# Kernel optimization log

Hardware: AMD Instinct MI355X
Metric: run time of the kernel (lower is better)

## Reference

```python
import jax, jax.numpy as jnp
import numpy as np
import math

B, C, H, W = 16, 1, 1536, 1536


def setup_inputs() -> dict:
    key = jax.random.key(0)
    x = jax.random.normal(key, (B, C, H, W), dtype=jnp.float32)
    return {"inputs": x}


def _remove_nan(v):
    # utils.remove_nan: replace NaNs with zeros
    return jnp.where(jnp.isnan(v), jnp.zeros_like(v), v)


def reference(inputs):
    # Vectorized over batch; tf.map_fn applied axes 1,2 per-sample, which are
    # axes 2,3 (H, W) of the full (B, C, H, W) tensor.
    grad = lambda m, ax: jnp.roll(m, 1, axis=ax) - m
    p = grad(inputs, 2)          # d/dH
    q = grad(inputs, 3)          # d/dW
    r = grad(p, 2)               # d2/dH2
    s = grad(p, 3)               # d2/dHdW
    t = grad(q, 3)               # d2/dW2

    one_pq = 1.0 + p * p + q * q
    # mean curvature
    Hc = _remove_nan(-((1.0 + q * q) * r - 2.0 * p * q * s + (1.0 + p * p) * t)
                     / (2.0 * jnp.sqrt(one_pq ** 3)))
    # gaussian curvature
    Kc = _remove_nan((r * t - s * s) / (one_pq ** 2))

    root = jnp.sqrt(Hc * Hc - Kc)
    k_min = _remove_nan(Hc - root)
    k_max = _remove_nan(Hc + root)

    si = _remove_nan((2.0 / math.pi) * jnp.arctan((k_max + k_min) / (k_max - k_min)))
    return si
```

## Files before the change

### kernel.cpp

```cpp
#include <hip/hip_runtime.h>
#include <cmath>

#define B_ 16
#define H_ 1536
#define W_ 1536

typedef float v4f __attribute__((ext_vector_type(4)));

__global__ __launch_bounds__(384) void ShapeIndex_kernel(
        const float* __restrict__ x, float* __restrict__ out) {
#pragma clang fp contract(off)
    const int hraw = blockIdx.x;
    const int h  = (hraw & 7) * (H_ / 8) + (hraw >> 3);
    const int b  = blockIdx.y;
    const int w  = threadIdx.x * 4;

    const float* plane = x + (size_t)b * (H_ * W_);
    const int hm1 = (h == 0) ? (H_ - 1) : (h - 1);
    const int hm2 = (h <= 1) ? (h + H_ - 2) : (h - 2);

    const float4 vc = *(const float4*)(plane + h   * W_ + w);
    const float4 v1 = *(const float4*)(plane + hm1 * W_ + w);
    const float4 v2 = *(const float4*)(plane + hm2 * W_ + w);

    const int wm1 = (w == 0) ? (W_ - 1) : (w - 1);
    const int wm2 = (w == 0) ? (W_ - 2) : (w - 2);
    const float L0  = plane[h   * W_ + wm1];
    const float L1  = plane[h   * W_ + wm2];
    const float Lh1 = plane[hm1 * W_ + wm1];

    const v4f xc    = {vc.x, vc.y, vc.z, vc.w};
    const v4f xh1   = {v1.x, v1.y, v1.z, v1.w};
    const v4f xh2   = {v2.x, v2.y, v2.z, v2.w};
    const v4f xw1   = {L0,  vc.x, vc.y, vc.z};
    const v4f xw2   = {L1,  L0,  vc.x, vc.y};
    const v4f xh1w1 = {Lh1, v1.x, v1.y, v1.z};

    const v4f p    = xh1   - xc;
    const v4f q    = xw1   - xc;
    const v4f p_up = xh2   - xh1;
    const v4f p_lf = xh1w1 - xw1;
    const v4f q_lf = xw2   - xw1;
    const v4f r = p_up - p;
    const v4f s = p_lf - p;
    const v4f t = q_lf - q;

    const v4f pp = p * p;
    const v4f qq = q * q;
    const v4f one_pq = (1.0f + pp) + qq;
    const v4f A = ((1.0f + qq) * r - ((2.0f * p) * q) * s) + (1.0f + pp) * t;
    const v4f numk = r * t - s * s;

    v4f rsqv;
#pragma unroll
    for (int j = 0; j < 4; ++j)
        rsqv[j] = __builtin_amdgcn_rsqf(one_pq[j]);
    const v4f i2 = rsqv * rsqv;
    const v4f i3 = i2 * rsqv;
    const v4f i4 = i2 * i2;
    const v4f halfA = -0.5f * A;
    v4f Hc = halfA * i3;
    v4f Kc = numk * i4;
    const v4f HH = Hc * Hc;
    v4f disc = HH - Kc;

    v4f mag;
#pragma unroll
    for (int j = 0; j < 4; ++j) mag[j] = HH[j] + __builtin_fabsf(Kc[j]);
    const v4f thr = mag * 0x1p-16f;
    bool need[4];
    bool any = false;
#pragma unroll
    for (int j = 0; j < 4; ++j) {
        need[j] = __builtin_fabsf(disc[j]) <= thr[j];
        any |= need[j];
    }
    if (__builtin_expect(any, 0)) {
#pragma unroll
        for (int j = 0; j < 4; ++j) if (need[j]) {
            const float sqj  = one_pq[j] * one_pq[j];
            const float cubj = sqj * one_pq[j];
            const float se  = __builtin_sqrtf(cubj);
            const float hce = -(A[j] / (2.0f * se));
            const float kce = numk[j] / sqj;
            Hc[j]   = hce;
            disc[j] = hce * hce - kce;
        }
    }

    v4f root;
#pragma unroll
    for (int j = 0; j < 4; ++j) root[j] = __builtin_amdgcn_sqrtf(disc[j]);

    v4f u;
    bool big[4];
#pragma unroll
    for (int j = 0; j < 4; ++j) {
        const float aH = __builtin_fabsf(Hc[j]);
        big[j] = aH > root[j];
        const float mn = big[j] ? root[j] : aH;
        const float mx = big[j] ? aH : root[j];
        u[j] = mn * __builtin_amdgcn_rcpf(mx);
    }

    const v4f x2 = u * u;
    const v4f C5 = -0.01172120f, C4 = 0.05265332f, C3 = -0.11643287f,
              C2 = 0.19354346f,  C1 = -0.33262347f, C0 = 0.99997726f;
    v4f pl = __builtin_elementwise_fma(x2, C5, C4);
    pl = __builtin_elementwise_fma(x2, pl, C3);
    pl = __builtin_elementwise_fma(x2, pl, C2);
    pl = __builtin_elementwise_fma(x2, pl, C1);
    pl = __builtin_elementwise_fma(x2, pl, C0);
    const v4f a    = u * pl;
    const v4f asub = 1.57079632679489662f - a;

    v4f rs;
#pragma unroll
    for (int j = 0; j < 4; ++j)
        rs[j] = __builtin_copysignf(big[j] ? asub[j] : a[j], Hc[j]);
    const v4f siv = 0.63661977236758134f * rs;

    float res[4];
#pragma unroll
    for (int j = 0; j < 4; ++j)
        res[j] = (siv[j] == siv[j]) ? siv[j] : 0.0f;

    *(float4*)(out + (size_t)b * (H_ * W_) + h * W_ + w) =
        make_float4(res[0], res[1], res[2], res[3]);
}

extern "C" void kernel_launch(void* const* d_in, const int* in_sizes, int n_in,
                              void* d_out, int out_size, void* d_ws, size_t ws_size,
                              hipStream_t stream) {
    const float* x = (const float*)d_in[0];
    float* out = (float*)d_out;
    dim3 grid(H_, B_);
    dim3 block(384);
    ShapeIndex_kernel<<<grid, block, 0, stream>>>(x, out);
}
```

Baseline: 255.8 us.

## Process four rows per block to reuse vertical stencil loads

Each block now computes four consecutive output rows, loading six input rows once into registers and sharing them across the rows' stencils, and the grid shrinks by four. This cuts redundant global loads (previously each row reloaded its two upper neighbours plus the scalar left-halo values), which should help a memory-bound stencil. The cost is more registers per thread and fewer blocks in flight, which may lower occupancy and latency hiding; the scalar halo loads are still unvectorised.

```diff
diff --git a/kernel.cpp b/kernel.cpp
--- a/kernel.cpp
+++ b/kernel.cpp
@@ -10,123 +10,141 @@
 __global__ __launch_bounds__(384) void ShapeIndex_kernel(
         const float* __restrict__ x, float* __restrict__ out) {
 #pragma clang fp contract(off)
-    const int hraw = blockIdx.x;
-    const int h  = (hraw & 7) * (H_ / 8) + (hraw >> 3);
+    const int graw = blockIdx.x;
+    const int g  = (graw & 7) * (384 / 8) + (graw >> 3);
+    const int h0 = g * 4;
     const int b  = blockIdx.y;
     const int w  = threadIdx.x * 4;
 
     const float* plane = x + (size_t)b * (H_ * W_);
-    const int hm1 = (h == 0) ? (H_ - 1) : (h - 1);
-    const int hm2 = (h <= 1) ? (h + H_ - 2) : (h - 2);
+    const int rm1 = (h0 == 0) ? H_ - 1 : h0 - 1;
+    const int rm2 = (h0 == 0) ? H_ - 2 : h0 - 2;
 
-    const float4 vc = *(const float4*)(plane + h   * W_ + w);
-    const float4 v1 = *(const float4*)(plane + hm1 * W_ + w);
-    const float4 v2 = *(const float4*)(plane + hm2 * W_ + w);
+    const int rows[6] = {rm2, rm1, h0, h0 + 1, h0 + 2, h0 + 3};
+
+    float4 R[6];
+#pragma unroll
+    for (int i = 0; i < 6; ++i)
+        R[i] = *(const float4*)(plane + (size_t)rows[i] * W_ + w);
 
     const int wm1 = (w == 0) ? (W_ - 1) : (w - 1);
     const int wm2 = (w == 0) ? (W_ - 2) : (w - 2);
-    const float L0  = plane[h   * W_ + wm1];
-    const float L1  = plane[h   * W_ + wm2];
-    const float Lh1 = plane[hm1 * W_ + wm1];
+    float Lw1[6], Lw2[6];
+#pragma unroll
+    for (int i = 1; i < 6; ++i) Lw1[i] = plane[(size_t)rows[i] * W_ + wm1];
+#pragma unroll
+    for (int i = 2; i < 6; ++i) Lw2[i] = plane[(size_t)rows[i] * W_ + wm2];
 
-    const v4f xc    = {vc.x, vc.y, vc.z, vc.w};
-    const v4f xh1   = {v1.x, v1.y, v1.z, v1.w};
-    const v4f xh2   = {v2.x, v2.y, v2.z, v2.w};
-    const v4f xw1   = {L0,  vc.x, vc.y, vc.z};
-    const v4f xw2   = {L1,  L0,  vc.x, vc.y};
-    const v4f xh1w1 = {Lh1, v1.x, v1.y, v1.z};
+    float* const oplane = out + (size_t)b * (H_ * W_);
 
-    const v4f p    = xh1   - xc;
-    const v4f q    = xw1   - xc;
-    const v4f p_up = xh2   - xh1;
-    const v4f p_lf = xh1w1 - xw1;
-    const v4f q_lf = xw2   - xw1;
-    const v4f r = p_up - p;
-    const v4f s = p_lf - p;
-    const v4f t = q_lf - q;
+#pragma unroll
+    for (int rr = 0; rr < 4; ++rr) {
+        const float4 vc = R[2 + rr];
+        const float4 v1 = R[1 + rr];
+        const float4 v2 = R[0 + rr];
+        const float L0  = Lw1[2 + rr];
+        const float L1  = Lw2[2 + rr];
+        const float Lh1 = Lw1[1 + rr];
 
-    const v4f pp = p * p;
-    const v4f qq = q * q;
-    const v4f one_pq = (1.0f + pp) + qq;
-    const v4f A = ((1.0f + qq) * r - ((2.0f * p) * q) * s) + (1.0f + pp) * t;
-    const v4f numk = r * t - s * s;
+        const v4f xc    = {vc.x, vc.y, vc.z, vc.w};
+        const v4f xh1   = {v1.x, v1.y, v1.z, v1.w};
+        const v4f xh2   = {v2.x, v2.y, v2.z, v2.w};
+        const v4f xw1   = {L0,  vc.x, vc.y, vc.z};
+        const v4f xw2   = {L1,  L0,  vc.x, vc.y};
+        const v4f xh1w1 = {Lh1, v1.x, v1.y, v1.z};
 
-    v4f rsqv;
+        const v4f p    = xh1   - xc;
+        const v4f q    = xw1   - xc;
+        const v4f p_up = xh2   - xh1;
+        const v4f p_lf = xh1w1 - xw1;
+        const v4f q_lf = xw2   - xw1;
+        const v4f r = p_up - p;
+        const v4f s = p_lf - p;
+        const v4f t = q_lf - q;
+
+        const v4f pp = p * p;
+        const v4f qq = q * q;
+        const v4f one_pq = (1.0f + pp) + qq;
+        const v4f A = ((1.0f + qq) * r - ((2.0f * p) * q) * s) + (1.0f + pp) * t;
+        const v4f numk = r * t - s * s;
+
+        v4f rsqv;
 #pragma unroll
-    for (int j = 0; j < 4; ++j)
-        rsqv[j] = __builtin_amdgcn_rsqf(one_pq[j]);
-    const v4f i2 = rsqv * rsqv;
-    const v4f i3 = i2 * rsqv;
-    const v4f i4 = i2 * i2;
-    const v4f halfA = -0.5f * A;
-    v4f Hc = halfA * i3;
-    v4f Kc = numk * i4;
-    const v4f HH = Hc * Hc;
-    v4f disc = HH - Kc;
+        for (int j = 0; j < 4; ++j)
+            rsqv[j] = __builtin_amdgcn_rsqf(one_pq[j]);
+        const v4f i2 = rsqv * rsqv;
+        const v4f i3 = i2 * rsqv;
+        const v4f i4 = i2 * i2;
+        const v4f halfA = -0.5f * A;
+        v4f Hc = halfA * i3;
+        v4f Kc = numk * i4;
+        const v4f HH = Hc * Hc;
+        v4f disc = HH - Kc;
 
-    v4f mag;
+        v4f mag;
 #pragma unroll
-    for (int j = 0; j < 4; ++j) mag[j] = HH[j] + __builtin_fabsf(Kc[j]);
-    const v4f thr = mag * 0x1p-16f;
-    bool need[4];
-    bool any = false;
+        for (int j = 0; j < 4; ++j) mag[j] = HH[j] + __builtin_fabsf(Kc[j]);
+        const v4f thr = mag * 0x1p-16f;
+        bool need[4];
+        bool any = false;
 #pragma unroll
-    for (int j = 0; j < 4; ++j) {
-        need[j] = __builtin_fabsf(disc[j]) <= thr[j];
-        any |= need[j];
+        for (int j = 0; j < 4; ++j) {
+            need[j] = __builtin_fabsf(disc[j]) <= thr[j];
+            any |= need[j];
+        }
+        if (__builtin_expect(any, 0)) {
+#pragma unroll
+            for (int j = 0; j < 4; ++j) if (need[j]) {
+                const float sqj  = one_pq[j] * one_pq[j];
+                const float cubj = sqj * one_pq[j];
+                const float se  = __builtin_sqrtf(cubj);
+                const float hce = -(A[j] / (2.0f * se));
+                const float kce = numk[j] / sqj;
+                Hc[j]   = hce;
+                disc[j] = hce * hce - kce;
+            }
+        }
+
+        v4f root;
+#pragma unroll
+        for (int j = 0; j < 4; ++j) root[j] = __builtin_amdgcn_sqrtf(disc[j]);
+
+        v4f u;
+        bool big[4];
+#pragma unroll
+        for (int j = 0; j < 4; ++j) {
+            const float aH = __builtin_fabsf(Hc[j]);
+            big[j] = aH > root[j];
+            const float mn = big[j] ? root[j] : aH;
+            const float mx = big[j] ? aH : root[j];
+            u[j] = mn * __builtin_amdgcn_rcpf(mx);
+        }
+
+        const v4f x2 = u * u;
+        const v4f C5 = -0.01172120f, C4 = 0.05265332f, C3 = -0.11643287f,
+                  C2 = 0.19354346f,  C1 = -0.33262347f, C0 = 0.99997726f;
+        v4f pl = __builtin_elementwise_fma(x2, C5, C4);
+        pl = __builtin_elementwise_fma(x2, pl, C3);
+        pl = __builtin_elementwise_fma(x2, pl, C2);
+        pl = __builtin_elementwise_fma(x2, pl, C1);
+        pl = __builtin_elementwise_fma(x2, pl, C0);
+        const v4f a    = u * pl;
+        const v4f asub = 1.57079632679489662f - a;
+
+        v4f rs;
+#pragma unroll
+        for (int j = 0; j < 4; ++j)
+            rs[j] = __builtin_copysignf(big[j] ? asub[j] : a[j], Hc[j]);
+        const v4f siv = 0.63661977236758134f * rs;
+
+        float res[4];
+#pragma unroll
+        for (int j = 0; j < 4; ++j)
+            res[j] = (siv[j] == siv[j]) ? siv[j] : 0.0f;
+
+        *(float4*)(oplane + (size_t)(h0 + rr) * W_ + w) =
+            make_float4(res[0], res[1], res[2], res[3]);
     }
-    if (__builtin_expect(any, 0)) {
-#pragma unroll
-        for (int j = 0; j < 4; ++j) if (need[j]) {
-            const float sqj  = one_pq[j] * one_pq[j];
-            const float cubj = sqj * one_pq[j];
-            const float se  = __builtin_sqrtf(cubj);
-            const float hce = -(A[j] / (2.0f * se));
-            const float kce = numk[j] / sqj;
-            Hc[j]   = hce;
-            disc[j] = hce * hce - kce;
-        }
-    }
-
-    v4f root;
-#pragma unroll
-    for (int j = 0; j < 4; ++j) root[j] = __builtin_amdgcn_sqrtf(disc[j]);
-
-    v4f u;
-    bool big[4];
-#pragma unroll
-    for (int j = 0; j < 4; ++j) {
-        const float aH = __builtin_fabsf(Hc[j]);
-        big[j] = aH > root[j];
-        const float mn = big[j] ? root[j] : aH;
-        const float mx = big[j] ? aH : root[j];
-        u[j] = mn * __builtin_amdgcn_rcpf(mx);
-    }
-
-    const v4f x2 = u * u;
-    const v4f C5 = -0.01172120f, C4 = 0.05265332f, C3 = -0.11643287f,
-              C2 = 0.19354346f,  C1 = -0.33262347f, C0 = 0.99997726f;
-    v4f pl = __builtin_elementwise_fma(x2, C5, C4);
-    pl = __builtin_elementwise_fma(x2, pl, C3);
-    pl = __builtin_elementwise_fma(x2, pl, C2);
-    pl = __builtin_elementwise_fma(x2, pl, C1);
-    pl = __builtin_elementwise_fma(x2, pl, C0);
-    const v4f a    = u * pl;
-    const v4f asub = 1.57079632679489662f - a;
-
-    v4f rs;
-#pragma unroll
-    for (int j = 0; j < 4; ++j)
-        rs[j] = __builtin_copysignf(big[j] ? asub[j] : a[j], Hc[j]);
-    const v4f siv = 0.63661977236758134f * rs;
-
-    float res[4];
-#pragma unroll
-    for (int j = 0; j < 4; ++j)
-        res[j] = (siv[j] == siv[j]) ? siv[j] : 0.0f;
-
-    *(float4*)(out + (size_t)b * (H_ * W_) + h * W_ + w) =
-        make_float4(res[0], res[1], res[2], res[3]);
 }
 
 extern "C" void kernel_launch(void* const* d_in, const int* in_sizes, int n_in,
@@ -134,7 +152,7 @@
                               hipStream_t stream) {
     const float* x = (const float*)d_in[0];
     float* out = (float*)d_out;
-    dim3 grid(H_, B_);
+    dim3 grid(H_ / 4, B_);
     dim3 block(384);
     ShapeIndex_kernel<<<grid, block, 0, stream>>>(x, out);
 }
```

New measurement: 256.9 us. Within noise of the previous version (+0.4%).
